# Optimization experiments

Measured on AMD Instinct MI355X. Metric: run time of the kernel, lower is better.

Reference implementation:

```python
import jax, jax.numpy as jnp
import numpy as np

NUM_LETTERS = 33
EMB = 64
HID = 512
KPT = 21
CRD = 3
SEQ = 100
IN0 = EMB * 2 + KPT * CRD * 2  # 254


def setup_inputs() -> dict:
    key = jax.random.key(0)
    ks = jax.random.split(key, 16)
    B = 4096
    s = 0.05
    return {
        "start_letters": jax.random.randint(ks[0], (B,), 0, NUM_LETTERS, dtype=jnp.int32),
        "end_letters": jax.random.randint(ks[1], (B,), 0, NUM_LETTERS, dtype=jnp.int32),
        "start_coords": jax.random.normal(ks[2], (B, KPT * CRD), jnp.float32),
        "end_coords": jax.random.normal(ks[3], (B, KPT * CRD), jnp.float32),
        "emb": jax.random.normal(ks[4], (NUM_LETTERS, EMB), jnp.float32) * s,
        "W_ih0": jax.random.normal(ks[5], (4 * HID, IN0), jnp.float32) * s,
        "W_hh0": jax.random.normal(ks[6], (4 * HID, HID), jnp.float32) * s,
        "b_ih0": jax.random.normal(ks[7], (4 * HID,), jnp.float32) * s,
        "b_hh0": jax.random.normal(ks[8], (4 * HID,), jnp.float32) * s,
        "W_ih1": jax.random.normal(ks[9], (4 * HID, HID), jnp.float32) * s,
        "W_hh1": jax.random.normal(ks[10], (4 * HID, HID), jnp.float32) * s,
        "b_ih1": jax.random.normal(ks[11], (4 * HID,), jnp.float32) * s,
        "b_hh1": jax.random.normal(ks[12], (4 * HID,), jnp.float32) * s,
        "fc_W": jax.random.normal(ks[13], (KPT * CRD, HID), jnp.float32) * s,
        "fc_b": jax.random.normal(ks[14], (KPT * CRD,), jnp.float32) * s,
    }


def _lstm_cell(pre, c):
    # PyTorch gate order: input, forget, cell(g), output
    i, f, g, o = jnp.split(pre, 4, axis=-1)
    c_new = jax.nn.sigmoid(f) * c + jax.nn.sigmoid(i) * jnp.tanh(g)
    h_new = jax.nn.sigmoid(o) * jnp.tanh(c_new)
    return h_new, c_new


def reference(start_letters, end_letters, start_coords, end_coords,
              emb, W_ih0, W_hh0, b_ih0, b_hh0, W_ih1, W_hh1, b_ih1, b_hh1,
              fc_W, fc_b):
    # combined input, constant across timesteps: [B, 254]
    x = jnp.concatenate([emb[start_letters], emb[end_letters],
                         start_coords, end_coords], axis=-1)
    B = x.shape[0]
    # layer-0 input projection is constant per step -> hoist out of the scan
    x0 = x @ W_ih0.T + b_ih0 + b_hh0  # [B, 4H]
    b1 = b_ih1 + b_hh1

    def step(carry, _):
        h0, c0, h1, c1 = carry
        h0, c0 = _lstm_cell(x0 + h0 @ W_hh0.T, c0)
        h1, c1 = _lstm_cell(h0 @ W_ih1.T + b1 + h1 @ W_hh1.T, c1)
        y = h1 @ fc_W.T + fc_b  # [B, 63]
        return (h0, c0, h1, c1), y

    z = jnp.zeros((B, HID), x.dtype)
    _, ys = jax.lax.scan(step, (z, z, z, z), None, length=SEQ)  # [T, B, 63]
    # -> [B, keypoints, coords, T]
    return jnp.moveaxis(ys, 0, -1).reshape(B, KPT, CRD, SEQ)
```

## Files before the change

kernel.cpp:

```cpp
#include <hip/hip_runtime.h>


#define HIDN  512
#define SEQL  100
#define BATCH 4096
#define NB    8
#define BR    128

typedef _Float16 f16;
typedef _Float16 half8 __attribute__((ext_vector_type(8)));
typedef float    f32x4 __attribute__((ext_vector_type(4)));
typedef unsigned int u32x4 __attribute__((ext_vector_type(4)));

#define OFF_XCAT   0ul
#define OFF_X0PT   (OFF_XCAT + 256ul*4096*4)
#define OFF_WP0    (OFF_X0PT + 2048ul*4096*4)
#define OFF_WP1I   (OFF_WP0  + 2048ul*512*2)
#define OFF_WP1H   (OFF_WP1I + 2048ul*512*2)
#define OFF_FCW    (OFF_WP1H + 2048ul*512*2)
#define OFF_B1P    (OFF_FCW  + 64ul*512*2)
#define OFF_H0     (OFF_B1P  + 2048ul*4)
#define OFF_H1     (OFF_H0   + 2ul*4096*512*2)
#define OFF_FLAGS  (OFF_H1   + 2ul*4096*512*2)
#define FLAG_BYTES (32ul*128*4)

__device__ __forceinline__ int orow(int pr){
  return (((pr>>6)&3)<<9) | ((pr>>8)<<6) | (pr&63);
}
__device__ __forceinline__ float sigm(float x){ return 1.f/(1.f + __expf(-x)); }
__device__ __forceinline__ float tanhx(float x){ return 1.f - 2.f/(1.f + __expf(2.f*x)); }
__device__ __forceinline__ f32x4 splat4(float v){ f32x4 r; r[0]=v; r[1]=v; r[2]=v; r[3]=v; return r; }

__global__ __launch_bounds__(256) void k_xcat(
    const int* __restrict__ sl, const int* __restrict__ el,
    const float* __restrict__ sc, const float* __restrict__ ec,
    const float* __restrict__ emb, float* __restrict__ xcatT)
{
  int b = blockIdx.x*256 + threadIdx.x;
  int c = blockIdx.y;
  float v = 0.f;
  if      (c < 64 ) v = emb[sl[b]*64 + c];
  else if (c < 128) v = emb[el[b]*64 + (c-64)];
  else if (c < 191) v = sc[b*63 + (c-128)];
  else if (c < 254) v = ec[b*63 + (c-191)];
  xcatT[c*4096 + b] = v;
}

__global__ __launch_bounds__(256) void k_pack(
    const float* __restrict__ Whh0, const float* __restrict__ Wih1,
    const float* __restrict__ Whh1, const float* __restrict__ fcW,
    const float* __restrict__ bih1, const float* __restrict__ bhh1,
    f16* __restrict__ Wp0, f16* __restrict__ Wp1i, f16* __restrict__ Wp1h,
    f16* __restrict__ fcWp, float* __restrict__ b1p)
{
  int row = blockIdx.x, tid = threadIdx.x;
  if (row < 6144){
    int m  = row >> 11;
    int pr = row & 2047;
    const float* src = (m==0) ? Whh0 : (m==1) ? Wih1 : Whh1;
    f16* dst = (m==0) ? Wp0 : (m==1) ? Wp1i : Wp1h;
    int orig = orow(pr);
    dst[pr*512 + tid      ] = (f16)src[orig*512 + tid      ];
    dst[pr*512 + tid + 256] = (f16)src[orig*512 + tid + 256];
  } else if (row < 6208){
    int n = row - 6144;
    float v0 = (n < 63) ? fcW[n*512 + tid      ] : 0.f;
    float v1 = (n < 63) ? fcW[n*512 + tid + 256] : 0.f;
    fcWp[n*512 + tid] = (f16)v0; fcWp[n*512 + tid + 256] = (f16)v1;
  } else {
    int j = row - 6208;
    int orig = (((tid>>6)&3)<<9) | (j<<6) | (tid&63);
    b1p[j*256 + tid] = bih1[orig] + bhh1[orig];
  }
}

__global__ __launch_bounds__(256) void k_x0(
    const float* __restrict__ xcatT, const float* __restrict__ Wih0,
    const float* __restrict__ bih0, const float* __restrict__ bhh0,
    float* __restrict__ x0pT)
{
  int pr0 = blockIdx.x * 16;
  int b   = blockIdx.y * 256 + threadIdx.x;
  float a[16];
#pragma unroll
  for (int i=0;i<16;i++) a[i] = 0.f;
  for (int k=0;k<254;k++){
    float xv = xcatT[k*4096 + b];
#pragma unroll
    for (int i=0;i<16;i++)
      a[i] = fmaf(xv, Wih0[orow(pr0+i)*254 + k], a[i]);
  }
#pragma unroll
  for (int i=0;i<16;i++){
    int orig = orow(pr0+i);
    x0pT[(size_t)(pr0+i)*4096 + b] = a[i] + bih0[orig] + bhh0[orig];
  }
}

__global__ __launch_bounds__(512, 2) void k_lstm(
    const float* __restrict__ x0pT, const f16* __restrict__ Wp0,
    const f16* __restrict__ Wp1i, const f16* __restrict__ Wp1h,
    const f16* __restrict__ fcWp, const float* __restrict__ b1p,
    const float* __restrict__ fcb, f16* __restrict__ h0buf,
    f16* __restrict__ h1buf, unsigned int* __restrict__ flags,
    float* __restrict__ out)
{
  __shared__ f16 Ach[2][128*40];
  __shared__ f16 Bch[2][256*40];

  const int tid  = threadIdx.x;
  const int blk  = blockIdx.x;
  const int j    = blk & 7;
  const int team = blk >> 3;
  const int b0   = team * BR;
  const int w = tid >> 6, wr = w >> 2, wc = w & 3;
  const int lane = tid & 63, quad = lane >> 4, lc = lane & 15;
  const int ucol = wc*16 + lc;
  const bool des = (j == (team & 7));

  const f16* Wb0  = Wp0  + (size_t)(j*256)*512;
  const f16* Wb1i = Wp1i + (size_t)(j*256)*512;
  const f16* Wb1h = Wp1h + (size_t)(j*256)*512;

  float b1v[4];
#pragma unroll
  for (int g=0; g<4; g++) b1v[g] = b1p[j*256 + g*64 + ucol];
  const float fcbv = (ucol < 63) ? fcb[ucol] : 0.f;

  f32x4 c0[4], c1[4];
#pragma unroll
  for (int mt=0; mt<4; mt++){ c0[mt] = splat4(0.f); c1[mt] = splat4(0.f); }

  const int srA = tid >> 2;
  const int ssg = (tid & 3) * 8;
  unsigned int* tflags = flags + team*128;

  auto barrier = [&](int idx){
    __syncthreads();
    if (tid == 0){
      __threadfence();
      __hip_atomic_fetch_add(&tflags[idx], 1u, __ATOMIC_RELAXED, __HIP_MEMORY_SCOPE_AGENT);
      while (__hip_atomic_load(&tflags[idx], __ATOMIC_RELAXED, __HIP_MEMORY_SCOPE_AGENT) < (unsigned)NB)
        __builtin_amdgcn_s_sleep(4);
      __threadfence();
    }
    __syncthreads();
  };

  auto GEMM = [&](int nch, auto&& Aat, auto&& Bat, f32x4 (&acc)[4][4],
                  bool dofc, f32x4* fca, int fck0){
    u32x4 ra, rb0, rb1;
    auto ld = [&](int kc){
      const f16* Ap = Aat(kc);
      const f16* Bp = Bat(kc);
      ra  = *(const u32x4*)(Ap + (size_t)srA*HIDN + ssg);
      rb0 = *(const u32x4*)(Bp + (size_t)srA*HIDN + ssg);
      rb1 = *(const u32x4*)(Bp + (size_t)(srA+128)*HIDN + ssg);
    };
    auto st = [&](int kc){
      int bu = kc & 1;
      *(u32x4*)&Ach[bu][srA*40 + ssg]        = ra;
      *(u32x4*)&Bch[bu][srA*40 + ssg]        = rb0;
      *(u32x4*)&Bch[bu][(srA+128)*40 + ssg]  = rb1;
    };
    ld(0); st(0);
    if (nch > 1) ld(1);
    for (int kc=0; kc<nch; kc++){
      __syncthreads();
      if (kc+1 < nch){
        st(kc+1);
        if (kc+2 < nch) ld(kc+2);
      }
      const int bu = kc & 1;
      half8 af[4];
#pragma unroll
      for (int mt=0; mt<4; mt++)
        af[mt] = *(const half8*)&Ach[bu][(wr*64 + mt*16 + lc)*40 + quad*8];
#pragma unroll
      for (int g=0; g<4; g++){
        half8 bf = *(const half8*)&Bch[bu][(g*64 + ucol)*40 + quad*8];
#pragma unroll
        for (int mt=0; mt<4; mt++)
          acc[g][mt] = __builtin_amdgcn_mfma_f32_16x16x32_f16(af[mt], bf, acc[g][mt], 0, 0, 0);
      }
      if (dofc && kc >= fck0){
        half8 fb = *(const half8*)(fcWp + (size_t)ucol*HIDN + (kc-fck0)*32 + quad*8);
#pragma unroll
        for (int mt=0; mt<4; mt++)
          fca[mt] = __builtin_amdgcn_mfma_f32_16x16x32_f16(af[mt], fb, fca[mt], 0, 0, 0);
      }
    }
  };

  for (int t=0; t<SEQL; t++){
    const int p  = t & 1;
    const int pp = (t-1) & 1;
    const f16* h0rd = h0buf + (size_t)pp*BATCH*HIDN + (size_t)b0*HIDN;
    const f16* h1rd = h1buf + (size_t)pp*BATCH*HIDN + (size_t)b0*HIDN;
    f16* h0wr = h0buf + (size_t)p*BATCH*HIDN;
    f16* h1wr = h1buf + (size_t)p*BATCH*HIDN;

    f32x4 acc[4][4];
#pragma unroll
    for (int g=0; g<4; g++)
#pragma unroll
      for (int mt=0; mt<4; mt++)
        acc[g][mt] = *(const f32x4*)(x0pT + (size_t)(j*256 + g*64 + ucol)*4096
                                     + b0 + wr*64 + mt*16 + quad*4);
    if (t > 0){
      GEMM(16, [&](int kc){ return h0rd + kc*32; },
               [&](int kc){ return Wb0  + kc*32; },
           acc, false, (f32x4*)nullptr, 0);
    }
#pragma unroll
    for (int mt=0; mt<4; mt++){
#pragma unroll
      for (int r=0; r<4; r++){
        float iv = sigm(acc[0][mt][r]);
        float fv = sigm(acc[1][mt][r]);
        float gv = tanhx(acc[2][mt][r]);
        float ov = sigm(acc[3][mt][r]);
        float cn = fv*c0[mt][r] + iv*gv;
        c0[mt][r] = cn;
        float hn = ov * tanhx(cn);
        int row = wr*64 + mt*16 + quad*4 + r;
        h0wr[(size_t)(b0+row)*HIDN + j*64 + ucol] = (f16)hn;
      }
    }
    barrier(t);

    const f16* h0cur = h0buf + (size_t)p*BATCH*HIDN + (size_t)b0*HIDN;
#pragma unroll
    for (int g=0; g<4; g++)
#pragma unroll
      for (int mt=0; mt<4; mt++)
        acc[g][mt] = splat4(b1v[g]);
    f32x4 fca[4];
#pragma unroll
    for (int mt=0; mt<4; mt++) fca[mt] = splat4(fcbv);

    if (t > 0){
      GEMM(32, [&](int kc){ return kc < 16 ? h0cur + kc*32 : h1rd  + (kc-16)*32; },
               [&](int kc){ return kc < 16 ? Wb1i  + kc*32 : Wb1h + (kc-16)*32; },
           acc, des, fca, 16);
      if (des && ucol < 63){
#pragma unroll
        for (int mt=0; mt<4; mt++)
#pragma unroll
          for (int r=0; r<4; r++){
            int row = wr*64 + mt*16 + quad*4 + r;
            out[((b0+row)*63 + ucol)*100 + (t-1)] = fca[mt][r];
          }
      }
    } else {
      GEMM(16, [&](int kc){ return h0cur + kc*32; },
               [&](int kc){ return Wb1i  + kc*32; },
           acc, false, (f32x4*)nullptr, 0);
    }
#pragma unroll
    for (int mt=0; mt<4; mt++){
#pragma unroll
      for (int r=0; r<4; r++){
        float iv = sigm(acc[0][mt][r]);
        float fv = sigm(acc[1][mt][r]);
        float gv = tanhx(acc[2][mt][r]);
        float ov = sigm(acc[3][mt][r]);
        float cn = fv*c1[mt][r] + iv*gv;
        c1[mt][r] = cn;
        float hn = ov * tanhx(cn);
        int row = wr*64 + mt*16 + quad*4 + r;
        h1wr[(size_t)(b0+row)*HIDN + j*64 + ucol] = (f16)hn;
      }
    }
  }

  barrier(SEQL);
  if (des){
    const f16* h1last = h1buf + (size_t)1*BATCH*HIDN + (size_t)b0*HIDN;
    f32x4 fca[4];
#pragma unroll
    for (int mt=0; mt<4; mt++) fca[mt] = splat4(fcbv);
    for (int kc=0; kc<16; kc++){
      __syncthreads();
      *(u32x4*)&Ach[0][srA*40 + ssg] = *(const u32x4*)(h1last + (size_t)srA*HIDN + kc*32 + ssg);
      __syncthreads();
      half8 af[4];
#pragma unroll
      for (int mt=0; mt<4; mt++)
        af[mt] = *(const half8*)&Ach[0][(wr*64 + mt*16 + lc)*40 + quad*8];
      half8 fb = *(const half8*)(fcWp + (size_t)ucol*HIDN + kc*32 + quad*8);
#pragma unroll
      for (int mt=0; mt<4; mt++)
        fca[mt] = __builtin_amdgcn_mfma_f32_16x16x32_f16(af[mt], fb, fca[mt], 0, 0, 0);
    }
    if (ucol < 63){
#pragma unroll
      for (int mt=0; mt<4; mt++)
#pragma unroll
        for (int r=0; r<4; r++){
          int row = wr*64 + mt*16 + quad*4 + r;
          out[((b0+row)*63 + ucol)*100 + 99] = fca[mt][r];
        }
    }
  }
}

extern "C" void kernel_launch(void* const* d_in, const int* in_sizes, int n_in,
                              void* d_out, int out_size, void* d_ws, size_t ws_size,
                              hipStream_t stream)
{
  const int*   sl   = (const int*)  d_in[0];
  const int*   el   = (const int*)  d_in[1];
  const float* sc   = (const float*)d_in[2];
  const float* ec   = (const float*)d_in[3];
  const float* emb  = (const float*)d_in[4];
  const float* Wih0 = (const float*)d_in[5];
  const float* Whh0 = (const float*)d_in[6];
  const float* bih0 = (const float*)d_in[7];
  const float* bhh0 = (const float*)d_in[8];
  const float* Wih1 = (const float*)d_in[9];
  const float* Whh1 = (const float*)d_in[10];
  const float* bih1 = (const float*)d_in[11];
  const float* bhh1 = (const float*)d_in[12];
  const float* fcW  = (const float*)d_in[13];
  const float* fcb  = (const float*)d_in[14];

  char* ws = (char*)d_ws;
  float* xcatT = (float*)(ws + OFF_XCAT);
  float* x0pT  = (float*)(ws + OFF_X0PT);
  f16*   Wp0   = (f16*)  (ws + OFF_WP0);
  f16*   Wp1i  = (f16*)  (ws + OFF_WP1I);
  f16*   Wp1h  = (f16*)  (ws + OFF_WP1H);
  f16*   fcWp  = (f16*)  (ws + OFF_FCW);
  float* b1p   = (float*)(ws + OFF_B1P);
  f16*   h0b   = (f16*)  (ws + OFF_H0);
  f16*   h1b   = (f16*)  (ws + OFF_H1);
  unsigned int* flags = (unsigned int*)(ws + OFF_FLAGS);

  hipMemsetAsync(flags, 0, FLAG_BYTES, stream);
  k_xcat<<<dim3(16, 256), 256, 0, stream>>>(sl, el, sc, ec, emb, xcatT);
  k_pack<<<6216, 256, 0, stream>>>(Whh0, Wih1, Whh1, fcW, bih1, bhh1,
                                   Wp0, Wp1i, Wp1h, fcWp, b1p);
  k_x0<<<dim3(128, 16), 256, 0, stream>>>(xcatT, Wih0, bih0, bhh0, x0pT);
  k_lstm<<<256, 512, 0, stream>>>(x0pT, Wp0, Wp1i, Wp1h, fcWp, b1p, fcb,
                                  h0b, h1b, flags, (float*)d_out);
}
```

Before: 8.272 ms.

## Load LSTM weights directly into registers, use coherent h loads, fp16 x0 projection

The recurrent GEMM no longer stages the weight tile through shared memory. Each lane now loads its B fragments straight from global memory into registers, and the A (hidden state) staging gets four LDS buffers with a two-chunk software pipeline. Hidden-state loads and stores use system-coherent sc0/sc1 instructions, which lets the barrier drop its threadfences in favour of a vmcnt wait. The hoisted x0 projection is stored in fp16 with its weights cached in LDS, trading some input precision for less bandwidth.

```diff
diff --git a/kernel.cpp b/kernel.cpp
--- a/kernel.cpp
+++ b/kernel.cpp
@@ -10,7 +10,6 @@
 typedef _Float16 f16;
 typedef _Float16 half8 __attribute__((ext_vector_type(8)));
 typedef float    f32x4 __attribute__((ext_vector_type(4)));
-typedef unsigned int u32x4 __attribute__((ext_vector_type(4)));
 
 #define OFF_XCAT   0ul
 #define OFF_X0PT   (OFF_XCAT + 256ul*4096*4)
@@ -30,6 +29,25 @@
 __device__ __forceinline__ float sigm(float x){ return 1.f/(1.f + __expf(-x)); }
 __device__ __forceinline__ float tanhx(float x){ return 1.f - 2.f/(1.f + __expf(2.f*x)); }
 __device__ __forceinline__ f32x4 splat4(float v){ f32x4 r; r[0]=v; r[1]=v; r[2]=v; r[3]=v; return r; }
+
+__device__ __forceinline__ unsigned int ld_coh_u32(const void* p){
+  unsigned int r;
+  asm volatile("global_load_dword %0, %1, off sc0 sc1"
+               : "=v"(r) : "v"(p) : "memory");
+  return r;
+}
+__device__ __forceinline__ void st_coh_u16(void* p, unsigned int d){
+  asm volatile("global_store_short %0, %1, off sc0 sc1"
+               :: "v"(p), "v"(d) : "memory");
+}
+__device__ __forceinline__ void wait_vm0(){
+  asm volatile("s_waitcnt vmcnt(0)" ::: "memory");
+}
+__device__ __forceinline__ unsigned int f16bits(float x){
+  union { f16 h; unsigned short s; } u;
+  u.h = (f16)x;
+  return (unsigned int)u.s;
+}
 
 __global__ __launch_bounds__(256) void k_xcat(
     const int* __restrict__ sl, const int* __restrict__ el,
@@ -77,36 +95,45 @@
 __global__ __launch_bounds__(256) void k_x0(
     const float* __restrict__ xcatT, const float* __restrict__ Wih0,
     const float* __restrict__ bih0, const float* __restrict__ bhh0,
-    float* __restrict__ x0pT)
-{
-  int pr0 = blockIdx.x * 16;
-  int b   = blockIdx.y * 256 + threadIdx.x;
-  float a[16];
-#pragma unroll
-  for (int i=0;i<16;i++) a[i] = 0.f;
-  for (int k=0;k<254;k++){
+    f16* __restrict__ x0ph)
+{
+  __shared__ float Wl[32*256];
+  __shared__ float bl[32];
+  const int tid = threadIdx.x;
+  const int pr0 = blockIdx.x * 32;
+  const int b   = blockIdx.y * 256 + tid;
+  for (int idx = tid; idx < 32*256; idx += 256){
+    int r = idx >> 8, k = idx & 255;
+    Wl[idx] = (k < 254) ? Wih0[orow(pr0+r)*254 + k] : 0.f;
+  }
+  if (tid < 32){
+    int orig = orow(pr0+tid);
+    bl[tid] = bih0[orig] + bhh0[orig];
+  }
+  __syncthreads();
+  float a[32];
+#pragma unroll
+  for (int r=0;r<32;r++) a[r] = 0.f;
+  for (int k=0; k<254; k++){
     float xv = xcatT[k*4096 + b];
 #pragma unroll
-    for (int i=0;i<16;i++)
-      a[i] = fmaf(xv, Wih0[orow(pr0+i)*254 + k], a[i]);
-  }
-#pragma unroll
-  for (int i=0;i<16;i++){
-    int orig = orow(pr0+i);
-    x0pT[(size_t)(pr0+i)*4096 + b] = a[i] + bih0[orig] + bhh0[orig];
-  }
+    for (int r=0;r<32;r++)
+      a[r] = fmaf(xv, Wl[r*256 + k], a[r]);
+  }
+#pragma unroll
+  for (int r=0;r<32;r++)
+    x0ph[(size_t)(pr0+r)*4096 + b] = (f16)(a[r] + bl[r]);
 }
 
 __global__ __launch_bounds__(512, 2) void k_lstm(
-    const float* __restrict__ x0pT, const f16* __restrict__ Wp0,
+    const f16* __restrict__ x0ph, const f16* __restrict__ Wp0,
     const f16* __restrict__ Wp1i, const f16* __restrict__ Wp1h,
     const f16* __restrict__ fcWp, const float* __restrict__ b1p,
     const float* __restrict__ fcb, f16* __restrict__ h0buf,
     f16* __restrict__ h1buf, unsigned int* __restrict__ flags,
     float* __restrict__ out)
 {
-  __shared__ f16 Ach[2][128*40];
-  __shared__ f16 Bch[2][256*40];
+  __shared__ __align__(16) f16 Ach[4][128*40];
 
   const int tid  = threadIdx.x;
   const int blk  = blockIdx.x;
@@ -121,6 +148,13 @@
   const f16* Wb0  = Wp0  + (size_t)(j*256)*512;
   const f16* Wb1i = Wp1i + (size_t)(j*256)*512;
   const f16* Wb1h = Wp1h + (size_t)(j*256)*512;
+  const f16* xb   = x0ph + (size_t)(j*256)*4096 + b0;
+
+  const int srA   = tid >> 2;
+  const int ssg   = (tid & 3) * 8;
+  const int Aoff  = srA*HIDN + ssg;
+  const int boffB = ucol*512 + quad*8;
+  unsigned int* tflags = flags + team*128;
 
   float b1v[4];
 #pragma unroll
@@ -131,66 +165,76 @@
 #pragma unroll
   for (int mt=0; mt<4; mt++){ c0[mt] = splat4(0.f); c1[mt] = splat4(0.f); }
 
-  const int srA = tid >> 2;
-  const int ssg = (tid & 3) * 8;
-  unsigned int* tflags = flags + team*128;
-
   auto barrier = [&](int idx){
+    wait_vm0();
     __syncthreads();
     if (tid == 0){
-      __threadfence();
       __hip_atomic_fetch_add(&tflags[idx], 1u, __ATOMIC_RELAXED, __HIP_MEMORY_SCOPE_AGENT);
       while (__hip_atomic_load(&tflags[idx], __ATOMIC_RELAXED, __HIP_MEMORY_SCOPE_AGENT) < (unsigned)NB)
         __builtin_amdgcn_s_sleep(4);
-      __threadfence();
     }
     __syncthreads();
   };
 
-  auto GEMM = [&](int nch, auto&& Aat, auto&& Bat, f32x4 (&acc)[4][4],
+  auto GEMM = [&](int nch, int wsw, const f16* A1, const f16* A2,
+                  const f16* W1, const f16* W2, f32x4 (&acc)[4][4],
                   bool dofc, f32x4* fca, int fck0){
-    u32x4 ra, rb0, rb1;
-    auto ld = [&](int kc){
-      const f16* Ap = Aat(kc);
-      const f16* Bp = Bat(kc);
-      ra  = *(const u32x4*)(Ap + (size_t)srA*HIDN + ssg);
-      rb0 = *(const u32x4*)(Bp + (size_t)srA*HIDN + ssg);
-      rb1 = *(const u32x4*)(Bp + (size_t)(srA+128)*HIDN + ssg);
+    unsigned int rA[4], rB[4];
+    auto ldp = [&](int kc, unsigned int* r){
+      const f16* p = (kc < wsw ? A1 + kc*32 : A2 + (kc-wsw)*32) + Aoff;
+      const unsigned int* q = (const unsigned int*)p;
+      r[0] = ld_coh_u32(q+0); r[1] = ld_coh_u32(q+1);
+      r[2] = ld_coh_u32(q+2); r[3] = ld_coh_u32(q+3);
     };
-    auto st = [&](int kc){
-      int bu = kc & 1;
-      *(u32x4*)&Ach[bu][srA*40 + ssg]        = ra;
-      *(u32x4*)&Bch[bu][srA*40 + ssg]        = rb0;
-      *(u32x4*)&Bch[bu][(srA+128)*40 + ssg]  = rb1;
+    auto stp = [&](int kc, const unsigned int* r){
+      unsigned int* d = (unsigned int*)&Ach[kc&3][srA*40 + ssg];
+      d[0]=r[0]; d[1]=r[1]; d[2]=r[2]; d[3]=r[3];
     };
-    ld(0); st(0);
-    if (nch > 1) ld(1);
-    for (int kc=0; kc<nch; kc++){
-      __syncthreads();
-      if (kc+1 < nch){
-        st(kc+1);
-        if (kc+2 < nch) ld(kc+2);
-      }
-      const int bu = kc & 1;
+    auto Bld = [&](int kc, half8* bf){
+      const f16* WB = (kc < wsw ? W1 + kc*32 : W2 + (kc-wsw)*32) + boffB;
+#pragma unroll
+      for (int g=0; g<4; g++) bf[g] = *(const half8*)(WB + g*32768);
+    };
+    auto comp = [&](int kc, const half8* bf){
+      const int bu = kc&3;
       half8 af[4];
 #pragma unroll
       for (int mt=0; mt<4; mt++)
         af[mt] = *(const half8*)&Ach[bu][(wr*64 + mt*16 + lc)*40 + quad*8];
 #pragma unroll
-      for (int g=0; g<4; g++){
-        half8 bf = *(const half8*)&Bch[bu][(g*64 + ucol)*40 + quad*8];
+      for (int g=0; g<4; g++)
 #pragma unroll
         for (int mt=0; mt<4; mt++)
-          acc[g][mt] = __builtin_amdgcn_mfma_f32_16x16x32_f16(af[mt], bf, acc[g][mt], 0, 0, 0);
-      }
+          acc[g][mt] = __builtin_amdgcn_mfma_f32_16x16x32_f16(af[mt], bf[g], acc[g][mt], 0, 0, 0);
       if (dofc && kc >= fck0){
-        half8 fb = *(const half8*)(fcWp + (size_t)ucol*HIDN + (kc-fck0)*32 + quad*8);
+        half8 fb = *(const half8*)(fcWp + boffB + (kc-fck0)*32);
 #pragma unroll
         for (int mt=0; mt<4; mt++)
           fca[mt] = __builtin_amdgcn_mfma_f32_16x16x32_f16(af[mt], fb, fca[mt], 0, 0, 0);
       }
+    };
+
+    half8 bfE[4], bfO[4];
+    ldp(0, rA); ldp(1, rB);
+    wait_vm0();
+    stp(0, rA); stp(1, rB);
+    ldp(2, rA); ldp(3, rB);
+    Bld(0, bfE);
+    for (int kc=0; kc<nch; kc+=2){
+      __syncthreads();
+      wait_vm0();
+      if (kc+2 < nch) stp(kc+2, rA);
+      if (kc+3 < nch) stp(kc+3, rB);
+      if (kc+4 < nch) ldp(kc+4, rA);
+      if (kc+5 < nch) ldp(kc+5, rB);
+      Bld(kc+1, bfO);
+      comp(kc, bfE);
+      if (kc+2 < nch) Bld(kc+2, bfE);
+      comp(kc+1, bfO);
     }
   };
+
+  f32x4 fcd[4];
 
   for (int t=0; t<SEQL; t++){
     const int p  = t & 1;
@@ -204,14 +248,14 @@
 #pragma unroll
     for (int g=0; g<4; g++)
 #pragma unroll
-      for (int mt=0; mt<4; mt++)
-        acc[g][mt] = *(const f32x4*)(x0pT + (size_t)(j*256 + g*64 + ucol)*4096
-                                     + b0 + wr*64 + mt*16 + quad*4);
-    if (t > 0){
-      GEMM(16, [&](int kc){ return h0rd + kc*32; },
-               [&](int kc){ return Wb0  + kc*32; },
-           acc, false, (f32x4*)nullptr, 0);
-    }
+      for (int mt=0; mt<4; mt++){
+        const f16* xp = xb + (size_t)(g*64 + ucol)*4096 + wr*64 + mt*16 + quad*4;
+        f32x4 a;
+        a[0]=(float)xp[0]; a[1]=(float)xp[1]; a[2]=(float)xp[2]; a[3]=(float)xp[3];
+        acc[g][mt] = a;
+      }
+    if (t > 0)
+      GEMM(16, 16, h0rd, h0rd, Wb0, Wb0, acc, false, fcd, 0);
 #pragma unroll
     for (int mt=0; mt<4; mt++){
 #pragma unroll
@@ -224,7 +268,7 @@
         c0[mt][r] = cn;
         float hn = ov * tanhx(cn);
         int row = wr*64 + mt*16 + quad*4 + r;
-        h0wr[(size_t)(b0+row)*HIDN + j*64 + ucol] = (f16)hn;
+        st_coh_u16(h0wr + (size_t)(b0+row)*HIDN + j*64 + ucol, f16bits(hn));
       }
     }
     barrier(t);
@@ -240,9 +284,7 @@
     for (int mt=0; mt<4; mt++) fca[mt] = splat4(fcbv);
 
     if (t > 0){
-      GEMM(32, [&](int kc){ return kc < 16 ? h0cur + kc*32 : h1rd  + (kc-16)*32; },
-               [&](int kc){ return kc < 16 ? Wb1i  + kc*32 : Wb1h + (kc-16)*32; },
-           acc, des, fca, 16);
+      GEMM(32, 16, h0cur, h1rd, Wb1i, Wb1h, acc, des, fca, 16);
       if (des && ucol < 63){
 #pragma unroll
         for (int mt=0; mt<4; mt++)
@@ -253,9 +295,7 @@
           }
       }
     } else {
-      GEMM(16, [&](int kc){ return h0cur + kc*32; },
-               [&](int kc){ return Wb1i  + kc*32; },
-           acc, false, (f32x4*)nullptr, 0);
+      GEMM(16, 16, h0cur, h0cur, Wb1i, Wb1i, acc, false, fcd, 0);
     }
 #pragma unroll
     for (int mt=0; mt<4; mt++){
@@ -269,7 +309,7 @@
         c1[mt][r] = cn;
         float hn = ov * tanhx(cn);
         int row = wr*64 + mt*16 + quad*4 + r;
-        h1wr[(size_t)(b0+row)*HIDN + j*64 + ucol] = (f16)hn;
+        st_coh_u16(h1wr + (size_t)(b0+row)*HIDN + j*64 + ucol, f16bits(hn));
       }
     }
   }
@@ -282,13 +322,20 @@
     for (int mt=0; mt<4; mt++) fca[mt] = splat4(fcbv);
     for (int kc=0; kc<16; kc++){
       __syncthreads();
-      *(u32x4*)&Ach[0][srA*40 + ssg] = *(const u32x4*)(h1last + (size_t)srA*HIDN + kc*32 + ssg);
+      const unsigned int* q = (const unsigned int*)(h1last + kc*32 + Aoff);
+      unsigned int r0 = ld_coh_u32(q+0);
+      unsigned int r1 = ld_coh_u32(q+1);
+      unsigned int r2 = ld_coh_u32(q+2);
+      unsigned int r3 = ld_coh_u32(q+3);
+      wait_vm0();
+      unsigned int* d = (unsigned int*)&Ach[0][srA*40 + ssg];
+      d[0]=r0; d[1]=r1; d[2]=r2; d[3]=r3;
       __syncthreads();
       half8 af[4];
 #pragma unroll
       for (int mt=0; mt<4; mt++)
         af[mt] = *(const half8*)&Ach[0][(wr*64 + mt*16 + lc)*40 + quad*8];
-      half8 fb = *(const half8*)(fcWp + (size_t)ucol*HIDN + kc*32 + quad*8);
+      half8 fb = *(const half8*)(fcWp + boffB + kc*32);
 #pragma unroll
       for (int mt=0; mt<4; mt++)
         fca[mt] = __builtin_amdgcn_mfma_f32_16x16x32_f16(af[mt], fb, fca[mt], 0, 0, 0);
@@ -327,7 +374,7 @@
 
   char* ws = (char*)d_ws;
   float* xcatT = (float*)(ws + OFF_XCAT);
-  float* x0pT  = (float*)(ws + OFF_X0PT);
+  f16*   x0ph  = (f16*)  (ws + OFF_X0PT);
   f16*   Wp0   = (f16*)  (ws + OFF_WP0);
   f16*   Wp1i  = (f16*)  (ws + OFF_WP1I);
   f16*   Wp1h  = (f16*)  (ws + OFF_WP1H);
@@ -341,7 +388,7 @@
   k_xcat<<<dim3(16, 256), 256, 0, stream>>>(sl, el, sc, ec, emb, xcatT);
   k_pack<<<6216, 256, 0, stream>>>(Whh0, Wih1, Whh1, fcW, bih1, bhh1,
                                    Wp0, Wp1i, Wp1h, fcWp, b1p);
-  k_x0<<<dim3(128, 16), 256, 0, stream>>>(xcatT, Wih0, bih0, bhh0, x0pT);
-  k_lstm<<<256, 512, 0, stream>>>(x0pT, Wp0, Wp1i, Wp1h, fcWp, b1p, fcb,
+  k_x0<<<dim3(64, 16), 256, 0, stream>>>(xcatT, Wih0, bih0, bhh0, x0ph);
+  k_lstm<<<256, 512, 0, stream>>>(x0ph, Wp0, Wp1i, Wp1h, fcWp, b1p, fcb,
                                   h0b, h1b, flags, (float*)d_out);
 }
```

New measurement: 20.42 ms. +146.8%, slower.
